# Performance work log

Measured on AMD Instinct MI355X. Metric: run time of the kernel, lower is better.

Reference implementation:

```python
import jax, jax.numpy as jnp
import numpy as np

B, S, E = 8, 4096, 768
NEG = jnp.float32(-1e30)


def setup_inputs() -> dict:
    key = jax.random.key(0)
    ks = jax.random.split(key, 9)
    full_ebd = jax.random.normal(ks[0], (B, S, E), dtype=jnp.float32)
    # first_idx in [64, S//2): end of question span (question tokens are 1..first_idx-1)
    first = jax.random.randint(ks[1], (B,), 64, S // 2)
    # second_idx in (first, S): end of context span (unused by the math but part of API)
    second = jax.random.randint(ks[2], (B,), S // 2 + 1, S)
    SEQ_idxes = jnp.stack([first, second], axis=1).astype(jnp.int64)
    w = 0.02
    Wq_w = jax.random.normal(ks[3], (E, E), dtype=jnp.float32) * w
    Wq_b = jax.random.normal(ks[4], (E,), dtype=jnp.float32) * w
    Wk_w = jax.random.normal(ks[5], (E, E), dtype=jnp.float32) * w
    Wk_b = jax.random.normal(ks[6], (E,), dtype=jnp.float32) * w
    Wv_w = jax.random.normal(ks[7], (E, E), dtype=jnp.float32) * w
    Wv_b = jax.random.normal(ks[8], (E,), dtype=jnp.float32) * w
    return {"full_ebd": full_ebd, "SEQ_idxes": SEQ_idxes,
            "Wq_w": Wq_w, "Wq_b": Wq_b, "Wk_w": Wk_w, "Wk_b": Wk_b,
            "Wv_w": Wv_w, "Wv_b": Wv_b}


def reference(full_ebd, SEQ_idxes, Wq_w, Wq_b, Wk_w, Wk_b, Wv_w, Wv_b):
    # Vectorized form of the ragged per-sample loop: queries attend to the
    # question tokens 1..first_idx-1 only; masking keys reproduces the slice.
    seq = full_ebd.shape[1]
    inv_sqrt_dk = jnp.float32(1.0 / np.sqrt(full_ebd.shape[-1]))
    Q = full_ebd @ Wq_w.T + Wq_b              # [B,S,E]
    K = full_ebd @ Wk_w.T + Wk_b              # [B,S,E]
    V = full_ebd @ Wv_w.T + Wv_b              # [B,S,E]
    first = SEQ_idxes[:, 0]                   # [B]
    j = jnp.arange(seq)
    key_mask = (j[None, :] >= 1) & (j[None, :] < first[:, None])  # [B,S]
    scores = jnp.einsum('bqe,bke->bqk', Q, K) * inv_sqrt_dk       # [B,S,S]
    scores = jnp.where(key_mask[:, None, :], scores, NEG)
    attn = jax.nn.softmax(scores, axis=-1)
    attn = attn * key_mask[:, None, :].astype(attn.dtype)  # exact zeros outside span
    H = jnp.einsum('bqk,bke->bqe', attn, V)   # [B,S,E]
    return H
```

## Files before the change

kernel.cpp:

```cpp
#include <hip/hip_runtime.h>
#include <hip/hip_bf16.h>
#include <cmath>

typedef __bf16 bf16x8 __attribute__((ext_vector_type(8)));
typedef __bf16 bf16x4 __attribute__((ext_vector_type(4)));
typedef float f32x4 __attribute__((ext_vector_type(4)));

#define GLOBAL_AS __attribute__((address_space(1)))
#define LDS_AS __attribute__((address_space(3)))

__device__ __forceinline__ void async_copy16(const void* g, void* l) {
    __builtin_amdgcn_global_load_lds((const GLOBAL_AS void*)g, (LDS_AS void*)l, 16, 0, 0);
}

__device__ inline int get_first(const int* __restrict__ seq, int b) {
    int stride = (seq[1] == 0) ? 4 : 2;
    return seq[b * stride];
}

__global__ __launch_bounds__(256) void cast_f32_bf16(const float* __restrict__ in,
                                                     __bf16* __restrict__ out, int n4) {
    int i = blockIdx.x * 256 + threadIdx.x;
    if (i >= n4) return;
    float4 v = ((const float4*)in)[i];
    bf16x4 o;
    o[0] = (__bf16)v.x; o[1] = (__bf16)v.y; o[2] = (__bf16)v.z; o[3] = (__bf16)v.w;
    ((bf16x4*)out)[i] = o;
}

__global__ __launch_bounds__(256) void cast3_f32_bf16(
    const float* __restrict__ a, const float* __restrict__ b, const float* __restrict__ c,
    __bf16* __restrict__ oa, __bf16* __restrict__ ob, __bf16* __restrict__ oc, int n4) {
    int i = blockIdx.x * 256 + threadIdx.x;
    if (i >= n4) return;
    const float* in = (blockIdx.y == 0) ? a : (blockIdx.y == 1) ? b : c;
    __bf16* out = (blockIdx.y == 0) ? oa : (blockIdx.y == 1) ? ob : oc;
    float4 v = ((const float4*)in)[i];
    bf16x4 o;
    o[0] = (__bf16)v.x; o[1] = (__bf16)v.y; o[2] = (__bf16)v.z; o[3] = (__bf16)v.w;
    ((bf16x4*)out)[i] = o;
}

__global__ __launch_bounds__(256) void zero_f32(float* __restrict__ p, int n4) {
    int i = blockIdx.x * 256 + threadIdx.x;
    if (i < n4) ((f32x4*)p)[i] = f32x4{0.f, 0.f, 0.f, 0.f};
}

template <int EPI>
__global__ __launch_bounds__(256) void gemm_bt(
    const __bf16* __restrict__ A, int lda, long strideA,
    const __bf16* __restrict__ B, int ldb, long strideB,
    const float* __restrict__ bias,
    void* __restrict__ Cv, int ldc, long strideC,
    int Kfix, const int* __restrict__ seq, int exit_mode, int k_mode,
    float cs, float* __restrict__ rowsum) {
    int z = blockIdx.z;
    int m0 = blockIdx.x * 128, n0 = blockIdx.y * 128;
    int first = seq ? get_first(seq, z) : 0;
    if (exit_mode == 1 && m0 >= first) return;
    if (exit_mode == 2 && n0 >= first) return;
    int K = k_mode ? ((first + 63) & ~63) : Kfix;

    __shared__ char As[16384];
    __shared__ char Bs[16384];

    int tid = threadIdx.x;
    int lane = tid & 63, wid = tid >> 6;
    int waveM = (wid & 1) << 6, waveN = (wid >> 1) << 6;
    int quad = lane >> 4, l16 = lane & 15;

    int r0 = tid >> 3;
    int c8 = (tid & 7) ^ (r0 & 7);
    const __bf16* Ag = A + (long)z * strideA + (long)(m0 + r0) * lda + c8 * 8;
    const __bf16* Bg = B + (long)z * strideB + (long)(n0 + r0) * ldb + c8 * 8;

    f32x4 acc[4][4] = {};
    int xorv = (l16 & 7) << 4;

    for (int k0 = 0; k0 < K; k0 += 64) {
        __syncthreads();
#pragma unroll
        for (int r = 0; r < 4; ++r) {
            async_copy16(Ag + (long)(r * 32) * lda + k0, As + (tid + r * 256) * 16);
            async_copy16(Bg + (long)(r * 32) * ldb + k0, Bs + (tid + r * 256) * 16);
        }
        __syncthreads();
#pragma unroll
        for (int s = 0; s < 2; ++s) {
            bf16x8 af[4], bfr[4];
#pragma unroll
            for (int i = 0; i < 4; ++i) {
                int chunk = (((s << 2) + quad) << 4) ^ xorv;
                af[i]  = *(const bf16x8*)(As + (waveM + i * 16 + l16) * 128 + chunk);
                bfr[i] = *(const bf16x8*)(Bs + (waveN + i * 16 + l16) * 128 + chunk);
            }
#pragma unroll
            for (int i = 0; i < 4; ++i)
#pragma unroll
                for (int j = 0; j < 4; ++j)
                    acc[i][j] = __builtin_amdgcn_mfma_f32_16x16x32_bf16(af[i], bfr[j], acc[i][j], 0, 0, 0);
        }
    }

    if (EPI == 0) {
        __bf16* C = (__bf16*)Cv + (long)z * strideC;
#pragma unroll
        for (int i = 0; i < 4; ++i) {
            int rowb = m0 + waveM + i * 16 + quad * 4;
#pragma unroll
            for (int j = 0; j < 4; ++j) {
                int col = n0 + waveN + j * 16 + l16;
                float bv_ = bias[col];
#pragma unroll
                for (int r = 0; r < 4; ++r)
                    C[(long)(rowb + r) * ldc + col] = (__bf16)(acc[i][j][r] + bv_);
            }
        }
    } else if (EPI == 1) {
        __bf16* C = (__bf16*)Cv + (long)z * strideC;
#pragma unroll
        for (int i = 0; i < 4; ++i) {
            int rowb = m0 + waveM + i * 16 + quad * 4;
#pragma unroll
            for (int j = 0; j < 4; ++j) {
                int col = n0 + waveN + j * 16 + l16;
                float bv_ = bias[col];
                bf16x4 o;
#pragma unroll
                for (int r = 0; r < 4; ++r) o[r] = (__bf16)(acc[i][j][r] + bv_);
                *(bf16x4*)&C[(long)col * ldc + rowb] = o;
            }
        }
    } else if (EPI == 2) {
        __bf16* C = (__bf16*)Cv + (long)z * strideC;
        float* rs = rowsum + (long)z * 4096;
#pragma unroll
        for (int i = 0; i < 4; ++i) {
            int rowb = m0 + waveM + i * 16 + quad * 4;
            float sum[4] = {0.f, 0.f, 0.f, 0.f};
#pragma unroll
            for (int j = 0; j < 4; ++j) {
                int col = n0 + waveN + j * 16 + l16;
                bool valid = (col >= 1) && (col < first);
#pragma unroll
                for (int r = 0; r < 4; ++r) {
                    float e = valid ? exp2f(acc[i][j][r] * cs) : 0.0f;
                    __bf16 pb = (__bf16)e;
                    C[(long)(rowb + r) * ldc + col] = pb;
                    sum[r] += (float)pb;
                }
            }
#pragma unroll
            for (int r = 0; r < 4; ++r) {
                float v = sum[r];
                v += __shfl_xor(v, 8); v += __shfl_xor(v, 4);
                v += __shfl_xor(v, 2); v += __shfl_xor(v, 1);
                if (l16 == 0) atomicAdd(&rs[rowb + r], v);
            }
        }
    } else {
        float* C = (float*)Cv + (long)z * strideC;
        const float* rs = rowsum + (long)z * 4096;
#pragma unroll
        for (int i = 0; i < 4; ++i) {
            int rowb = m0 + waveM + i * 16 + quad * 4;
            float inv[4];
#pragma unroll
            for (int r = 0; r < 4; ++r) inv[r] = 1.0f / rs[rowb + r];
#pragma unroll
            for (int j = 0; j < 4; ++j) {
                int col = n0 + waveN + j * 16 + l16;
#pragma unroll
                for (int r = 0; r < 4; ++r)
                    C[(long)(rowb + r) * ldc + col] = acc[i][j][r] * inv[r];
            }
        }
    }
}

extern "C" void kernel_launch(void* const* d_in, const int* in_sizes, int n_in,
                              void* d_out, int out_size, void* d_ws, size_t ws_size,
                              hipStream_t stream) {
    const int B = 8, S = 4096, E = 768, SK = 2048;
    const float* ebd  = (const float*)d_in[0];
    const int*   seq  = (const int*)d_in[1];
    const float* Wq_w = (const float*)d_in[2];
    const float* Wq_b = (const float*)d_in[3];
    const float* Wk_w = (const float*)d_in[4];
    const float* Wk_b = (const float*)d_in[5];
    const float* Wv_w = (const float*)d_in[6];
    const float* Wv_b = (const float*)d_in[7];
    float* out = (float*)d_out;

    char* p = (char*)d_ws;
    __bf16* ebd_bf = (__bf16*)p; p += (size_t)B * S * E * 2;
    __bf16* wq = (__bf16*)p;     p += (size_t)E * E * 2;
    __bf16* wk = (__bf16*)p;     p += (size_t)E * E * 2;
    __bf16* wv = (__bf16*)p;     p += (size_t)E * E * 2;
    __bf16* Qb = (__bf16*)p;     p += (size_t)B * S * E * 2;
    __bf16* Kb = (__bf16*)p;     p += (size_t)B * SK * E * 2;
    __bf16* VT = (__bf16*)p;     p += (size_t)B * E * SK * 2;
    __bf16* Pb = (__bf16*)p;     p += (size_t)B * S * SK * 2;
    float* rowsum = (float*)p;   p += (size_t)B * S * 4;

    zero_f32<<<B * S / 4 / 256, 256, 0, stream>>>(rowsum, B * S / 4);
    cast_f32_bf16<<<(B * S * E / 4 + 255) / 256, 256, 0, stream>>>(ebd, ebd_bf, B * S * E / 4);
    cast3_f32_bf16<<<dim3((E * E / 4 + 255) / 256, 3), 256, 0, stream>>>(
        Wq_w, Wk_w, Wv_w, wq, wk, wv, E * E / 4);

    float cs = (1.0f / sqrtf((float)E)) * 1.44269504088896f;

    gemm_bt<0><<<dim3(B * S / 128, E / 128, 1), 256, 0, stream>>>(
        ebd_bf, E, 0, wq, E, 0, Wq_b, Qb, E, 0, E, nullptr, 0, 0, 0.f, nullptr);
    gemm_bt<0><<<dim3(SK / 128, E / 128, B), 256, 0, stream>>>(
        ebd_bf, E, (long)S * E, wk, E, 0, Wk_b, Kb, E, (long)SK * E, E, seq, 1, 0, 0.f, nullptr);
    gemm_bt<1><<<dim3(SK / 128, E / 128, B), 256, 0, stream>>>(
        ebd_bf, E, (long)S * E, wv, E, 0, Wv_b, VT, SK, (long)E * SK, E, seq, 1, 0, 0.f, nullptr);
    gemm_bt<2><<<dim3(S / 128, SK / 128, B), 256, 0, stream>>>(
        Qb, E, (long)S * E, Kb, E, (long)SK * E, nullptr, Pb, SK, (long)S * SK, E, seq, 2, 0, cs, rowsum);
    gemm_bt<3><<<dim3(S / 128, E / 128, B), 256, 0, stream>>>(
        Pb, SK, (long)S * SK, VT, SK, (long)E * SK, nullptr, out, E, (long)S * E, 0, seq, 0, 1, 0.f, rowsum);
}
```

Baseline: 430.2 us.

## Use persistent atomic-counter tile schedulers and merge Q/K/V projections into one launch

Replaces the five grid-launched GEMMs with three persistent kernels that pull tile ids from atomic counters in the workspace, and fuses the Q, K and V projections into a single launch. Masked-out tiles are skipped without occupying a block slot, and ragged per-batch work is balanced dynamically across a fixed grid of 1280 blocks. The cost is an atomic plus two barriers per tile, and a zeroed counter area that piggybacks on the rowsum zeroing.

```diff
diff --git a/kernel.cpp b/kernel.cpp
--- a/kernel.cpp
+++ b/kernel.cpp
@@ -12,6 +12,11 @@
 __device__ __forceinline__ void async_copy16(const void* g, void* l) {
     __builtin_amdgcn_global_load_lds((const GLOBAL_AS void*)g, (LDS_AS void*)l, 16, 0, 0);
 }
+
+#define BB 8
+#define SS 4096
+#define EE 768
+#define SKK 2048
 
 __device__ inline int get_first(const int* __restrict__ seq, int b) {
     int stride = (seq[1] == 0) ? 4 : 2;
@@ -46,35 +51,22 @@
     if (i < n4) ((f32x4*)p)[i] = f32x4{0.f, 0.f, 0.f, 0.f};
 }
 
-template <int EPI>
-__global__ __launch_bounds__(256) void gemm_bt(
-    const __bf16* __restrict__ A, int lda, long strideA,
-    const __bf16* __restrict__ B, int ldb, long strideB,
-    const float* __restrict__ bias,
-    void* __restrict__ Cv, int ldc, long strideC,
-    int Kfix, const int* __restrict__ seq, int exit_mode, int k_mode,
-    float cs, float* __restrict__ rowsum) {
-    int z = blockIdx.z;
-    int m0 = blockIdx.x * 128, n0 = blockIdx.y * 128;
-    int first = seq ? get_first(seq, z) : 0;
-    if (exit_mode == 1 && m0 >= first) return;
-    if (exit_mode == 2 && n0 >= first) return;
-    int K = k_mode ? ((first + 63) & ~63) : Kfix;
-
-    __shared__ char As[16384];
-    __shared__ char Bs[16384];
-
+__device__ __forceinline__ void gemm_core(
+    const __bf16* __restrict__ A0, int lda,
+    const __bf16* __restrict__ B0, int ldb, int K,
+    char* As, char* Bs, f32x4 (&acc)[4][4]) {
     int tid = threadIdx.x;
     int lane = tid & 63, wid = tid >> 6;
     int waveM = (wid & 1) << 6, waveN = (wid >> 1) << 6;
     int quad = lane >> 4, l16 = lane & 15;
-
     int r0 = tid >> 3;
     int c8 = (tid & 7) ^ (r0 & 7);
-    const __bf16* Ag = A + (long)z * strideA + (long)(m0 + r0) * lda + c8 * 8;
-    const __bf16* Bg = B + (long)z * strideB + (long)(n0 + r0) * ldb + c8 * 8;
-
-    f32x4 acc[4][4] = {};
+    const __bf16* Ag = A0 + (long)r0 * lda + c8 * 8;
+    const __bf16* Bg = B0 + (long)r0 * ldb + c8 * 8;
+#pragma unroll
+    for (int i = 0; i < 4; ++i)
+#pragma unroll
+        for (int j = 0; j < 4; ++j) acc[i][j] = f32x4{0.f, 0.f, 0.f, 0.f};
     int xorv = (l16 & 7) << 4;
 
     for (int k0 = 0; k0 < K; k0 += 64) {
@@ -101,39 +93,108 @@
                     acc[i][j] = __builtin_amdgcn_mfma_f32_16x16x32_bf16(af[i], bfr[j], acc[i][j], 0, 0, 0);
         }
     }
-
-    if (EPI == 0) {
-        __bf16* C = (__bf16*)Cv + (long)z * strideC;
-#pragma unroll
-        for (int i = 0; i < 4; ++i) {
-            int rowb = m0 + waveM + i * 16 + quad * 4;
-#pragma unroll
-            for (int j = 0; j < 4; ++j) {
-                int col = n0 + waveN + j * 16 + l16;
-                float bv_ = bias[col];
-#pragma unroll
-                for (int r = 0; r < 4; ++r)
-                    C[(long)(rowb + r) * ldc + col] = (__bf16)(acc[i][j][r] + bv_);
-            }
-        }
-    } else if (EPI == 1) {
-        __bf16* C = (__bf16*)Cv + (long)z * strideC;
-#pragma unroll
-        for (int i = 0; i < 4; ++i) {
-            int rowb = m0 + waveM + i * 16 + quad * 4;
-#pragma unroll
-            for (int j = 0; j < 4; ++j) {
-                int col = n0 + waveN + j * 16 + l16;
-                float bv_ = bias[col];
-                bf16x4 o;
-#pragma unroll
-                for (int r = 0; r < 4; ++r) o[r] = (__bf16)(acc[i][j][r] + bv_);
-                *(bf16x4*)&C[(long)col * ldc + rowb] = o;
-            }
-        }
-    } else if (EPI == 2) {
-        __bf16* C = (__bf16*)Cv + (long)z * strideC;
-        float* rs = rowsum + (long)z * 4096;
+}
+
+
+__global__ __launch_bounds__(256) void proj_qkv(
+    const __bf16* __restrict__ ebd,
+    const __bf16* __restrict__ wq, const __bf16* __restrict__ wk, const __bf16* __restrict__ wv,
+    const float* __restrict__ bq, const float* __restrict__ bk, const float* __restrict__ bv,
+    __bf16* __restrict__ Qb, __bf16* __restrict__ Kb, __bf16* __restrict__ VT,
+    const int* __restrict__ seq, int* __restrict__ ctr) {
+    __shared__ char As[16384];
+    __shared__ char Bs[16384];
+    __shared__ int s_id;
+    int tid = threadIdx.x;
+    int lane = tid & 63, wid = tid >> 6;
+    int waveM = (wid & 1) << 6, waveN = (wid >> 1) << 6;
+    int quad = lane >> 4, l16 = lane & 15;
+
+    for (;;) {
+        __syncthreads();
+        if (tid == 0) s_id = atomicAdd(ctr, 1);
+        __syncthreads();
+        int id = s_id;
+        if (id >= 3072) return;
+
+        int which, m0, n0, z;
+        if (id < 1536) {
+            which = 0; m0 = (id & 31) << 7; n0 = ((id >> 5) % 6) << 7; z = id / 192;
+        } else {
+            int rel = id - 1536;
+            which = 1 + rel / 768; rel %= 768;
+            m0 = (rel & 15) << 7; n0 = ((rel >> 4) % 6) << 7; z = rel / 96;
+            if (m0 >= get_first(seq, z)) continue;
+        }
+        const __bf16* W = (which == 0) ? wq : (which == 1) ? wk : wv;
+        const float* bias = (which == 0) ? bq : (which == 1) ? bk : bv;
+
+        f32x4 acc[4][4];
+        gemm_core(ebd + (long)z * SS * EE + (long)m0 * EE, EE, W + (long)n0 * EE, EE,
+                  EE, As, Bs, acc);
+
+        if (which == 2) {
+            __bf16* C = VT + (long)z * EE * SKK;
+#pragma unroll
+            for (int i = 0; i < 4; ++i) {
+                int rowb = m0 + waveM + i * 16 + quad * 4;
+#pragma unroll
+                for (int j = 0; j < 4; ++j) {
+                    int col = n0 + waveN + j * 16 + l16;
+                    float bv_ = bias[col];
+                    bf16x4 o;
+#pragma unroll
+                    for (int r = 0; r < 4; ++r) o[r] = (__bf16)(acc[i][j][r] + bv_);
+                    *(bf16x4*)&C[(long)col * SKK + rowb] = o;
+                }
+            }
+        } else {
+            __bf16* C = (which == 0) ? Qb + (long)z * SS * EE : Kb + (long)z * SKK * EE;
+#pragma unroll
+            for (int i = 0; i < 4; ++i) {
+                int rowb = m0 + waveM + i * 16 + quad * 4;
+#pragma unroll
+                for (int j = 0; j < 4; ++j) {
+                    int col = n0 + waveN + j * 16 + l16;
+                    float bv_ = bias[col];
+#pragma unroll
+                    for (int r = 0; r < 4; ++r)
+                        C[(long)(rowb + r) * EE + col] = (__bf16)(acc[i][j][r] + bv_);
+                }
+            }
+        }
+    }
+}
+
+__global__ __launch_bounds__(256) void scores_k(
+    const __bf16* __restrict__ Qb, const __bf16* __restrict__ Kb,
+    __bf16* __restrict__ Pb, const int* __restrict__ seq,
+    float* __restrict__ rowsum, int* __restrict__ ctr) {
+    __shared__ char As[16384];
+    __shared__ char Bs[16384];
+    __shared__ int s_id;
+    int tid = threadIdx.x;
+    int lane = tid & 63, wid = tid >> 6;
+    int waveM = (wid & 1) << 6, waveN = (wid >> 1) << 6;
+    int quad = lane >> 4, l16 = lane & 15;
+    const float cs = 1.44269504088896f / 27.712812921102035f;
+
+    for (;;) {
+        __syncthreads();
+        if (tid == 0) s_id = atomicAdd(ctr, 1);
+        __syncthreads();
+        int id = s_id;
+        if (id >= 4096) return;
+        int m0 = (id & 31) << 7, n0 = ((id >> 5) & 15) << 7, z = id >> 9;
+        int first = get_first(seq, z);
+        if (n0 >= first) continue;
+
+        f32x4 acc[4][4];
+        gemm_core(Qb + (long)z * SS * EE + (long)m0 * EE, EE,
+                  Kb + (long)z * SKK * EE + (long)n0 * EE, EE, EE, As, Bs, acc);
+
+        __bf16* C = Pb + (long)z * SS * SKK;
+        float* rs = rowsum + (long)z * SS;
 #pragma unroll
         for (int i = 0; i < 4; ++i) {
             int rowb = m0 + waveM + i * 16 + quad * 4;
@@ -146,7 +207,7 @@
                 for (int r = 0; r < 4; ++r) {
                     float e = valid ? exp2f(acc[i][j][r] * cs) : 0.0f;
                     __bf16 pb = (__bf16)e;
-                    C[(long)(rowb + r) * ldc + col] = pb;
+                    C[(long)(rowb + r) * SKK + col] = pb;
                     sum[r] += (float)pb;
                 }
             }
@@ -158,9 +219,38 @@
                 if (l16 == 0) atomicAdd(&rs[rowb + r], v);
             }
         }
-    } else {
-        float* C = (float*)Cv + (long)z * strideC;
-        const float* rs = rowsum + (long)z * 4096;
+    }
+}
+
+__global__ __launch_bounds__(256) void pv_k(
+    const __bf16* __restrict__ Pb, const __bf16* __restrict__ VT,
+    float* __restrict__ out, const float* __restrict__ rowsum,
+    const int* __restrict__ seq, int* __restrict__ ctr) {
+    __shared__ char As[16384];
+    __shared__ char Bs[16384];
+    __shared__ int s_id;
+    int tid = threadIdx.x;
+    int lane = tid & 63, wid = tid >> 6;
+    int waveM = (wid & 1) << 6, waveN = (wid >> 1) << 6;
+    int quad = lane >> 4, l16 = lane & 15;
+
+    for (;;) {
+        __syncthreads();
+        if (tid == 0) s_id = atomicAdd(ctr, 1);
+        __syncthreads();
+        int id = s_id;
+        if (id >= 1536) return;
+        int m0 = (id & 31) << 7;
+        int t = id >> 5;
+        int n0 = (t % 6) << 7, z = t / 6;
+        int K = (get_first(seq, z) + 63) & ~63;
+
+        f32x4 acc[4][4];
+        gemm_core(Pb + (long)z * SS * SKK + (long)m0 * SKK, SKK,
+                  VT + (long)z * EE * SKK + (long)n0 * SKK, SKK, K, As, Bs, acc);
+
+        float* C = out + (long)z * SS * EE;
+        const float* rs = rowsum + (long)z * SS;
 #pragma unroll
         for (int i = 0; i < 4; ++i) {
             int rowb = m0 + waveM + i * 16 + quad * 4;
@@ -172,7 +262,7 @@
                 int col = n0 + waveN + j * 16 + l16;
 #pragma unroll
                 for (int r = 0; r < 4; ++r)
-                    C[(long)(rowb + r) * ldc + col] = acc[i][j][r] * inv[r];
+                    C[(long)(rowb + r) * EE + col] = acc[i][j][r] * inv[r];
             }
         }
     }
@@ -181,7 +271,7 @@
 extern "C" void kernel_launch(void* const* d_in, const int* in_sizes, int n_in,
                               void* d_out, int out_size, void* d_ws, size_t ws_size,
                               hipStream_t stream) {
-    const int B = 8, S = 4096, E = 768, SK = 2048;
+    const int B = BB, S = SS, E = EE, SK = SKK;
     const float* ebd  = (const float*)d_in[0];
     const int*   seq  = (const int*)d_in[1];
     const float* Wq_w = (const float*)d_in[2];
@@ -202,22 +292,16 @@
     __bf16* VT = (__bf16*)p;     p += (size_t)B * E * SK * 2;
     __bf16* Pb = (__bf16*)p;     p += (size_t)B * S * SK * 2;
     float* rowsum = (float*)p;   p += (size_t)B * S * 4;
-
-    zero_f32<<<B * S / 4 / 256, 256, 0, stream>>>(rowsum, B * S / 4);
+    int* ctrs = (int*)p;         p += 256;
+
+    zero_f32<<<(B * S / 4 + 64 + 255) / 256, 256, 0, stream>>>(rowsum, B * S / 4 + 64);
     cast_f32_bf16<<<(B * S * E / 4 + 255) / 256, 256, 0, stream>>>(ebd, ebd_bf, B * S * E / 4);
     cast3_f32_bf16<<<dim3((E * E / 4 + 255) / 256, 3), 256, 0, stream>>>(
         Wq_w, Wk_w, Wv_w, wq, wk, wv, E * E / 4);
 
-    float cs = (1.0f / sqrtf((float)E)) * 1.44269504088896f;
-
-    gemm_bt<0><<<dim3(B * S / 128, E / 128, 1), 256, 0, stream>>>(
-        ebd_bf, E, 0, wq, E, 0, Wq_b, Qb, E, 0, E, nullptr, 0, 0, 0.f, nullptr);
-    gemm_bt<0><<<dim3(SK / 128, E / 128, B), 256, 0, stream>>>(
-        ebd_bf, E, (long)S * E, wk, E, 0, Wk_b, Kb, E, (long)SK * E, E, seq, 1, 0, 0.f, nullptr);
-    gemm_bt<1><<<dim3(SK / 128, E / 128, B), 256, 0, stream>>>(
-        ebd_bf, E, (long)S * E, wv, E, 0, Wv_b, VT, SK, (long)E * SK, E, seq, 1, 0, 0.f, nullptr);
-    gemm_bt<2><<<dim3(S / 128, SK / 128, B), 256, 0, stream>>>(
-        Qb, E, (long)S * E, Kb, E, (long)SK * E, nullptr, Pb, SK, (long)S * SK, E, seq, 2, 0, cs, rowsum);
-    gemm_bt<3><<<dim3(S / 128, E / 128, B), 256, 0, stream>>>(
-        Pb, SK, (long)S * SK, VT, SK, (long)E * SK, nullptr, out, E, (long)S * E, 0, seq, 0, 1, 0.f, rowsum);
-}
+    const int NB = 1280;
+    proj_qkv<<<NB, 256, 0, stream>>>(ebd_bf, wq, wk, wv, Wq_b, Wk_b, Wv_b,
+                                     Qb, Kb, VT, seq, ctrs + 0);
+    scores_k<<<NB, 256, 0, stream>>>(Qb, Kb, Pb, seq, rowsum, ctrs + 1);
+    pv_k<<<NB, 256, 0, stream>>>(Pb, VT, out, rowsum, seq, ctrs + 2);
+}
```

Result: slower. 472.6 us (+9.9%).
